# Performance work log

Hardware: AMD Instinct MI355X
Metric: run time of the kernel (lower is better)

Reference implementation:

```python
import math
import jax, jax.numpy as jnp
import numpy as np

B, S, HID = 2, 2048, 4096
H, KV = 32, 8
D = HID // H  # 128


def setup_inputs() -> dict:
    key = jax.random.key(0)
    ks = jax.random.split(key, 6)
    std = 0.02
    x = jax.random.normal(ks[0], (B, S, HID), dtype=jnp.float32)
    # causal additive mask, broadcast over batch and heads
    neg = jnp.full((S, S), -1e9, dtype=jnp.float32)
    mask = jnp.triu(neg, k=1)[None, None, :, :]
    q_w = jax.random.normal(ks[1], (HID, HID), dtype=jnp.float32) * std
    k_w = jax.random.normal(ks[2], (KV * D, HID), dtype=jnp.float32) * std
    v_w = jax.random.normal(ks[3], (KV * D, HID), dtype=jnp.float32) * std
    o_w = jax.random.normal(ks[4], (HID, HID), dtype=jnp.float32) * std
    return {
        "x": x, "mask": mask,
        "q_w": q_w, "q_b": jnp.zeros((HID,), jnp.float32),
        "k_w": k_w, "k_b": jnp.zeros((KV * D,), jnp.float32),
        "v_w": v_w, "v_b": jnp.zeros((KV * D,), jnp.float32),
        "o_w": o_w, "o_b": jnp.zeros((HID,), jnp.float32),
    }


def reference(x, mask, q_w, q_b, k_w, k_b, v_w, v_b, o_w, o_b):
    b, s, _ = x.shape
    rep = H // KV
    # projections (torch Linear convention: y = x @ W^T + b)
    q = (x @ q_w.T + q_b).reshape(b, s, H, D)
    k = (x @ k_w.T + k_b).reshape(b, s, KV, D)
    v = (x @ v_w.T + v_b).reshape(b, s, KV, D)
    # GQA kv-head repeat via concat: q head i attends to kv head (i mod KV)
    k = jnp.concatenate([k] * rep, axis=2)  # [b, s, H, D]
    v = jnp.concatenate([v] * rep, axis=2)
    # [b, H, s, D]
    q = q.transpose(0, 2, 1, 3)
    k = k.transpose(0, 2, 1, 3)
    v = v.transpose(0, 2, 1, 3)
    scores = jnp.einsum("bhqd,bhkd->bhqk", q, k) / math.sqrt(D)
    scores = scores + mask
    w = jax.nn.softmax(scores, axis=-1)
    attn = jnp.einsum("bhqk,bhkd->bhqd", w, v)
    attn = attn.transpose(0, 2, 1, 3).reshape(b, s, HID)
    return attn @ o_w.T + o_b
```

## Files before the change

### kernel.cpp

```cpp
#include <hip/hip_runtime.h>
#include <hip/hip_bf16.h>
#include <cstdint>

typedef __attribute__((ext_vector_type(8))) short s8vec;
typedef __attribute__((ext_vector_type(4))) float f4vec;

#define DEV __device__ __forceinline__

constexpr int Bn = 2, Sn = 2048, HIDn = 4096, Hn = 32, KVn = 8, Dn = 128;

typedef const __attribute__((address_space(1))) void gvoid_t;
typedef __attribute__((address_space(3))) void lvoid_t;

DEV void async_ld16(const void* g, void* l) {
  __builtin_amdgcn_global_load_lds((gvoid_t*)g, (lvoid_t*)l, 16, 0, 0);
}

DEV f4vec mfma16(s8vec a, s8vec b, f4vec c) {
  return __builtin_amdgcn_mfma_f32_16x16x32_bf16(a, b, c, 0, 0, 0);
}

__global__ void cvt_all(const float* __restrict__ x, const float* __restrict__ qw,
                        const float* __restrict__ kw, const float* __restrict__ vw,
                        const float* __restrict__ ow,
                        __hip_bfloat16* __restrict__ xb, __hip_bfloat16* __restrict__ qwb,
                        __hip_bfloat16* __restrict__ kwb, __hip_bfloat16* __restrict__ vwb,
                        __hip_bfloat16* __restrict__ owb) {
  const int i = blockIdx.x * 256 + threadIdx.x;
  const float* src; __hip_bfloat16* dst; int off;
  if (i < 4194304)       { src = x;  dst = xb;  off = i; }
  else if (i < 8388608)  { src = qw; dst = qwb; off = i - 4194304; }
  else if (i < 9437184)  { src = kw; dst = kwb; off = i - 8388608; }
  else if (i < 10485760) { src = vw; dst = vwb; off = i - 9437184; }
  else                   { src = ow; dst = owb; off = i - 10485760; }
  float4 f = ((const float4*)src)[off];
  union { __hip_bfloat16 h[4]; uint2 u; } cv;
  cv.h[0] = __float2bfloat16(f.x);
  cv.h[1] = __float2bfloat16(f.y);
  cv.h[2] = __float2bfloat16(f.z);
  cv.h[3] = __float2bfloat16(f.w);
  ((uint2*)dst)[off] = cv.u;
}

template <typename EpiF>
DEV void gemm_bt_body(const __hip_bfloat16* A, const __hip_bfloat16* Bw, int K,
                      long m0, long n0, EpiF epi) {
  __shared__ __hip_bfloat16 As[128 * 32];
  __shared__ __hip_bfloat16 Bs[128 * 32];
  const int t = threadIdx.x;
  const int w = t >> 6, l = t & 63;
  const int lane15 = l & 15, quad = l >> 4;
  const int wm = (w >> 1) << 6, wn = (w & 1) << 6;

  f4vec acc[4][4] = {};

  const int srow = t >> 2;
  const int scol = (t & 3) << 3;
  const __hip_bfloat16* ag0 = A + (m0 + srow) * (long)K + scol;
  const __hip_bfloat16* ag1 = ag0 + 64 * (long)K;
  const __hip_bfloat16* bg0 = Bw + (n0 + srow) * (long)K + scol;
  const __hip_bfloat16* bg1 = bg0 + 64 * (long)K;
  char* lA = (char*)As + (w << 10);
  char* lB = (char*)Bs + (w << 10);
  const short* Ash = (const short*)As;
  const short* Bsh = (const short*)Bs;
  const int aoff = (wm + lane15) * 32 + (quad << 3);
  const int boff = (wn + lane15) * 32 + (quad << 3);

  for (int k0 = 0; k0 < K; k0 += 32) {
    __syncthreads();
    async_ld16(ag0 + k0, lA);
    async_ld16(ag1 + k0, lA + 4096);
    async_ld16(bg0 + k0, lB);
    async_ld16(bg1 + k0, lB + 4096);
    __syncthreads();
    s8vec af[4], bfr[4];
#pragma unroll
    for (int i = 0; i < 4; i++) {
      af[i] = *(const s8vec*)(Ash + aoff + i * 512);
      bfr[i] = *(const s8vec*)(Bsh + boff + i * 512);
    }
#pragma unroll
    for (int i = 0; i < 4; i++)
#pragma unroll
      for (int j = 0; j < 4; j++)
        acc[i][j] = mfma16(af[i], bfr[j], acc[i][j]);
  }
  epi(acc, wm, wn, lane15, quad);
}

__launch_bounds__(256, 2)
__global__ void gemm_qkv(const __hip_bfloat16* __restrict__ xb,
                         const __hip_bfloat16* __restrict__ qwb,
                         const __hip_bfloat16* __restrict__ kwb,
                         const __hip_bfloat16* __restrict__ vwb,
                         const float* __restrict__ qb, const float* __restrict__ kb,
                         const float* __restrict__ vb,
                         __hip_bfloat16* __restrict__ qh, __hip_bfloat16* __restrict__ kh,
                         __hip_bfloat16* __restrict__ vth) {
  const int bx = blockIdx.x;
  const long m0 = (long)blockIdx.y << 7;
  int mode; long n0;
  const __hip_bfloat16* Bw; const float* bias;
  if (bx < 32)      { mode = 0; Bw = qwb; bias = qb; n0 = (long)bx << 7; }
  else if (bx < 40) { mode = 1; Bw = kwb; bias = kb; n0 = (long)(bx - 32) << 7; }
  else              { mode = 2; Bw = vwb; bias = vb; n0 = (long)(bx - 40) << 7; }

  gemm_bt_body(xb, Bw, 4096, m0, n0,
    [&](f4vec (&acc)[4][4], int wm, int wn, int lane15, int quad) {
      float bv[4];
#pragma unroll
      for (int j = 0; j < 4; j++) bv[j] = bias[n0 + wn + j * 16 + lane15];
#pragma unroll
      for (int i = 0; i < 4; i++)
#pragma unroll
        for (int j = 0; j < 4; j++)
#pragma unroll
          for (int r = 0; r < 4; r++) {
            const long gm = m0 + wm + i * 16 + (quad << 2) + r;
            const long gn = n0 + wn + j * 16 + lane15;
            const float v = acc[i][j][r] + bv[j];
            const long bb = gm >> 11, ss = gm & 2047;
            const long hh = gn >> 7, dd = gn & 127;
            const __hip_bfloat16 hv = __float2bfloat16(v);
            if (mode == 0)
              qh[(((bb * Hn + hh) * Sn + ss) << 7) + dd] = hv;
            else if (mode == 1)
              kh[(((bb * KVn + hh) * Sn + ss) << 7) + dd] = hv;
            else
              vth[((bb * KVn + hh) * Dn + dd) * (long)Sn + ss] = hv;
          }
    });
}

__launch_bounds__(256, 2)
__global__ void gemm_out(const __hip_bfloat16* __restrict__ A,
                         const __hip_bfloat16* __restrict__ Bw,
                         const float* __restrict__ bias, float* __restrict__ Cout) {
  const long m0 = (long)blockIdx.y << 7;
  const long n0 = (long)blockIdx.x << 7;
  gemm_bt_body(A, Bw, 4096, m0, n0,
    [&](f4vec (&acc)[4][4], int wm, int wn, int lane15, int quad) {
      float bv[4];
#pragma unroll
      for (int j = 0; j < 4; j++) bv[j] = bias[n0 + wn + j * 16 + lane15];
#pragma unroll
      for (int i = 0; i < 4; i++)
#pragma unroll
        for (int j = 0; j < 4; j++)
#pragma unroll
          for (int r = 0; r < 4; r++) {
            const long gm = m0 + wm + i * 16 + (quad << 2) + r;
            const long gn = n0 + wn + j * 16 + lane15;
            Cout[gm * HIDn + gn] = acc[i][j][r] + bv[j];
          }
    });
}

__launch_bounds__(256, 2)
__global__ void attn_fused(const __hip_bfloat16* __restrict__ Qh,
                           const __hip_bfloat16* __restrict__ Kh,
                           const __hip_bfloat16* __restrict__ Vt,
                           __hip_bfloat16* __restrict__ Oa) {
  __shared__ __hip_bfloat16 Ks[2][64 * 128];
  __shared__ __hip_bfloat16 Vs[2][128 * 64];
  __shared__ __hip_bfloat16 Ps[4][32 * 64];

  const int pair = blockIdx.x;
  const int h = blockIdx.y;
  const int b = blockIdx.z;
  const int kv = h & 7;

  const int t = threadIdx.x, w = t >> 6, l = t & 63;
  const int lane15 = l & 15, quad = l >> 4;
  const int swz = lane15 & 7;

  const char* KgB = (const char*)(Kh + ((long)(b * KVn + kv)) * Sn * Dn);
  const char* VgB = (const char*)(Vt + ((long)(b * KVn + kv)) * Dn * (long)Sn);

  const int kc = (t & 15) ^ ((t >> 4) & 7);
  const char* kg_base = KgB + (t >> 4) * 256 + kc * 16;
  const int vc = (t & 7) ^ ((t >> 3) & 7);
  const char* vg_base = VgB + (t >> 3) * (size_t)(Sn * 2) + vc * 16;

  const short* Psh = (const short*)Ps[w];
  short* Psw = (short*)Ps[w];
  const float cscale = 0.08838834764831845f * 1.4426950408889634f;
  const float coff = -8.0f * 1.4426950408889634f;

  for (int ph = 0; ph < 2; ph++) {
    const int qt = ph ? (15 - pair) : pair;

    s8vec aq[2][4];
    {
      const short* Qgs = (const short*)(Qh + (((long)(b * Hn + h)) * Sn + qt * 128) * (long)Dn);
#pragma unroll
      for (int i = 0; i < 2; i++)
#pragma unroll
        for (int kk = 0; kk < 4; kk++)
          aq[i][kk] = *(const s8vec*)(Qgs + (w * 32 + i * 16 + lane15) * 128 + kk * 32 + (quad << 3));
    }
    float lsum[2][4] = {};
    f4vec acco[2][8] = {};

    __syncthreads();
    {
      char* lk = (char*)Ks[0] + (w << 10);
      char* lv = (char*)Vs[0] + (w << 10);
#pragma unroll
      for (int i = 0; i < 4; i++) async_ld16(kg_base + i * 4096, lk + i * 4096);
#pragma unroll
      for (int i = 0; i < 4; i++) async_ld16(vg_base + (size_t)i * 32 * Sn * 2, lv + i * 4096);
    }

    const int n_kt = 2 * qt + 2, full_kt = 2 * qt;
    for (int kt = 0; kt < n_kt; kt++) {
      const int cur = kt & 1;
      __syncthreads();
      if (kt + 1 < n_kt) {
        char* lk = (char*)Ks[cur ^ 1] + (w << 10);
        char* lv = (char*)Vs[cur ^ 1] + (w << 10);
        const char* kg = kg_base + (size_t)(kt + 1) * 16384;
        const char* vg = vg_base + (size_t)(kt + 1) * 128;
#pragma unroll
        for (int i = 0; i < 4; i++) async_ld16(kg + i * 4096, lk + i * 4096);
#pragma unroll
        for (int i = 0; i < 4; i++) async_ld16(vg + (size_t)i * 32 * Sn * 2, lv + i * 4096);
      }
      const short* Ksh = (const short*)Ks[cur];
      const short* Vsh = (const short*)Vs[cur];
      const bool need_mask = (kt >= full_kt);

#pragma unroll
      for (int j = 0; j < 4; j++) {
        f4vec as0 = {}, as1 = {};
#pragma unroll
        for (int kk = 0; kk < 4; kk++) {
          const s8vec bk = *(const s8vec*)(Ksh + (j * 16 + lane15) * 128 + (((quad + 4 * kk) ^ swz) << 3));
          as0 = mfma16(aq[0][kk], bk, as0);
          as1 = mfma16(aq[1][kk], bk, as1);
        }
        const int pc = j * 16 + lane15;
        const int kcol = kt * 64 + pc;
#pragma unroll
        for (int i = 0; i < 2; i++) {
#pragma unroll
          for (int r = 0; r < 4; r++) {
            const int pr = i * 16 + (quad << 2) + r;
            float sv = (i ? as1[r] : as0[r]) * cscale + coff;
            if (need_mask) {
              const int qr = qt * 128 + w * 32 + pr;
              if (kcol > qr) sv = -1000000.0f;
            }
            const float p = __builtin_amdgcn_exp2f(sv);
            lsum[i][r] += p;
            Psw[pr * 64 + ((((pc >> 3) ^ (pr & 7)) << 3) | (pc & 7))] =
                __bfloat16_as_short(__float2bfloat16(p));
          }
        }
      }
      asm volatile("s_waitcnt lgkmcnt(0)" ::: "memory");

#pragma unroll
      for (int kk = 0; kk < 2; kk++) {
        s8vec ap[2], bv8[8];
#pragma unroll
        for (int i = 0; i < 2; i++)
          ap[i] = *(const s8vec*)(Psh + (i * 16 + lane15) * 64 + (((quad + 4 * kk) ^ swz) << 3));
#pragma unroll
        for (int j = 0; j < 8; j++)
          bv8[j] = *(const s8vec*)(Vsh + (j * 16 + lane15) * 64 + (((quad + 4 * kk) ^ swz) << 3));
#pragma unroll
        for (int i = 0; i < 2; i++)
#pragma unroll
          for (int j = 0; j < 8; j++)
            acco[i][j] = mfma16(ap[i], bv8[j], acco[i][j]);
      }
    }

#pragma unroll
    for (int i = 0; i < 2; i++)
#pragma unroll
      for (int r = 0; r < 4; r++) {
        float s = lsum[i][r];
#pragma unroll
        for (int d = 1; d < 16; d <<= 1) s += __shfl_xor(s, d);
        lsum[i][r] = 1.0f / s;
      }
#pragma unroll
    for (int i = 0; i < 2; i++) {
#pragma unroll
      for (int r = 0; r < 4; r++) {
        const int row = qt * 128 + w * 32 + i * 16 + (quad << 2) + r;
        const long base = ((long)b * Sn + row) * HIDn + h * Dn;
#pragma unroll
        for (int j = 0; j < 8; j++)
          Oa[base + j * 16 + lane15] = __float2bfloat16(acco[i][j][r] * lsum[i][r]);
      }
    }
  }
}

extern "C" void kernel_launch(void* const* d_in, const int* in_sizes, int n_in,
                              void* d_out, int out_size, void* d_ws, size_t ws_size,
                              hipStream_t stream) {
  const float* x   = (const float*)d_in[0];
  const float* q_w = (const float*)d_in[2];
  const float* q_b = (const float*)d_in[3];
  const float* k_w = (const float*)d_in[4];
  const float* k_b = (const float*)d_in[5];
  const float* v_w = (const float*)d_in[6];
  const float* v_b = (const float*)d_in[7];
  const float* o_w = (const float*)d_in[8];
  const float* o_b = (const float*)d_in[9];

  char* ws = (char*)d_ws;
  size_t off = 0;
  auto nxt = [&](size_t bytes) { char* p = ws + off; off += bytes; return p; };
  __hip_bfloat16* xb  = (__hip_bfloat16*)nxt(33554432);
  __hip_bfloat16* qwb = (__hip_bfloat16*)nxt(33554432);
  __hip_bfloat16* kwb = (__hip_bfloat16*)nxt(8388608);
  __hip_bfloat16* vwb = (__hip_bfloat16*)nxt(8388608);
  __hip_bfloat16* owb = (__hip_bfloat16*)nxt(33554432);
  __hip_bfloat16* qh  = (__hip_bfloat16*)nxt(33554432);
  __hip_bfloat16* kh  = (__hip_bfloat16*)nxt(8388608);
  __hip_bfloat16* vth = (__hip_bfloat16*)nxt(8388608);
  __hip_bfloat16* at  = (__hip_bfloat16*)nxt(33554432);
  (void)ws_size; (void)in_sizes; (void)n_in; (void)out_size;

  cvt_all<<<57344, 256, 0, stream>>>(x, q_w, k_w, v_w, o_w, xb, qwb, kwb, vwb, owb);
  gemm_qkv<<<dim3(48, 32), 256, 0, stream>>>(xb, qwb, kwb, vwb, q_b, k_b, v_b, qh, kh, vth);
  attn_fused<<<dim3(8, 32, 2), 256, 0, stream>>>(qh, kh, vth, at);
  gemm_out<<<dim3(32, 32), 256, 0, stream>>>(at, owb, o_b, (float*)d_out);
}
```

Baseline: 743.2 us.

## Triple-buffer GEMM mainloop with 256x128 tiles, swizzled LDS and async prefetch

Reworks the shared GEMM body used by the QKV and output projections. It uses 256x128 block tiles with 8 waves and a K-step of 64, and stages operands into three LDS buffers via async global-to-LDS loads issued two iterations ahead. Synchronisation uses explicit vmcnt waits and a single barrier per step, and an XOR swizzle on LDS columns avoids bank conflicts. The aim is to hide global load latency and cut barrier overhead. In exchange, the large LDS footprint limits occupancy to one block per CU.

New measurement: 728.3 us. 2.0% less time.

```diff
diff --git a/kernel.cpp b/kernel.cpp
--- a/kernel.cpp
+++ b/kernel.cpp
@@ -45,51 +45,96 @@
 template <typename EpiF>
 DEV void gemm_bt_body(const __hip_bfloat16* A, const __hip_bfloat16* Bw, int K,
                       long m0, long n0, EpiF epi) {
-  __shared__ __hip_bfloat16 As[128 * 32];
-  __shared__ __hip_bfloat16 Bs[128 * 32];
+  __shared__ __hip_bfloat16 As[3][256 * 64];
+  __shared__ __hip_bfloat16 Bs[3][128 * 64];
   const int t = threadIdx.x;
   const int w = t >> 6, l = t & 63;
   const int lane15 = l & 15, quad = l >> 4;
-  const int wm = (w >> 1) << 6, wn = (w & 1) << 6;
+  const int wm = (w >> 1) << 6;
+  const int wn = (w & 1) << 6;
 
   f4vec acc[4][4] = {};
 
-  const int srow = t >> 2;
-  const int scol = (t & 3) << 3;
-  const __hip_bfloat16* ag0 = A + (m0 + srow) * (long)K + scol;
-  const __hip_bfloat16* ag1 = ag0 + 64 * (long)K;
-  const __hip_bfloat16* bg0 = Bw + (n0 + srow) * (long)K + scol;
-  const __hip_bfloat16* bg1 = bg0 + 64 * (long)K;
-  char* lA = (char*)As + (w << 10);
-  char* lB = (char*)Bs + (w << 10);
-  const short* Ash = (const short*)As;
-  const short* Bsh = (const short*)Bs;
-  const int aoff = (wm + lane15) * 32 + (quad << 3);
-  const int boff = (wn + lane15) * 32 + (quad << 3);
-
-  for (int k0 = 0; k0 < K; k0 += 32) {
-    __syncthreads();
-    async_ld16(ag0 + k0, lA);
-    async_ld16(ag1 + k0, lA + 4096);
-    async_ld16(bg0 + k0, lB);
-    async_ld16(bg1 + k0, lB + 4096);
-    __syncthreads();
-    s8vec af[4], bfr[4];
-#pragma unroll
-    for (int i = 0; i < 4; i++) {
-      af[i] = *(const s8vec*)(Ash + aoff + i * 512);
-      bfr[i] = *(const s8vec*)(Bsh + boff + i * 512);
-    }
+  const int col_e = ((l & 7) << 3) ^ (((l >> 5) & 1) << 4);
+  const __hip_bfloat16* agA = A + (m0 + w * 8 + (l >> 3)) * (long)K + col_e;
+  const __hip_bfloat16* agB = Bw + (n0 + w * 8 + (l >> 3)) * (long)K + col_e;
+  const long rowK64 = (long)K << 6;
+
+  auto stageA = [&](int buf, int kt, int i) {
+    async_ld16(agA + (long)i * rowK64 + ((long)kt << 6),
+               (char*)(As[buf]) + ((i * 8 + w) << 10));
+  };
+  auto stageB = [&](int buf, int kt, int i) {
+    async_ld16(agB + (long)i * rowK64 + ((long)kt << 6),
+               (char*)(Bs[buf]) + ((i * 8 + w) << 10));
+  };
+
+  const int colxor = (lane15 & 4) << 3;
+  const int cq = (quad << 4) ^ colxor;
+  int arow[4], brow[4];
+#pragma unroll
+  for (int i = 0; i < 4; i++) arow[i] = (wm + i * 16 + lane15) << 7;
+#pragma unroll
+  for (int j = 0; j < 4; j++) brow[j] = (wn + j * 16 + lane15) << 7;
+
+  const int NT = K >> 6;
+
+#pragma unroll
+  for (int i = 0; i < 4; i++) stageA(0, 0, i);
+#pragma unroll
+  for (int i = 0; i < 2; i++) stageB(0, 0, i);
+#pragma unroll
+  for (int i = 0; i < 4; i++) stageA(1, 1, i);
+#pragma unroll
+  for (int i = 0; i < 2; i++) stageB(1, 1, i);
+  asm volatile("s_waitcnt vmcnt(6)" ::: "memory");
+  __builtin_amdgcn_s_barrier();
+  __builtin_amdgcn_sched_barrier(0);
+
+  int bi = 0, nb = 2;
+  for (int tau = 0; tau < NT; ++tau) {
+    const char* Ab = (const char*)As[bi];
+    const char* Bb = (const char*)Bs[bi];
+    const bool st = (tau + 2) < NT;
+    s8vec af[4], bf4[4];
+
+#pragma unroll
+    for (int i = 0; i < 4; i++) af[i] = *(const s8vec*)(Ab + arow[i] + cq);
+#pragma unroll
+    for (int j = 0; j < 4; j++) bf4[j] = *(const s8vec*)(Bb + brow[j] + cq);
+    if (st) { stageA(nb, tau + 2, 0); stageA(nb, tau + 2, 1); stageB(nb, tau + 2, 0); }
+    __builtin_amdgcn_s_setprio(1);
 #pragma unroll
     for (int i = 0; i < 4; i++)
 #pragma unroll
-      for (int j = 0; j < 4; j++)
-        acc[i][j] = mfma16(af[i], bfr[j], acc[i][j]);
+      for (int j = 0; j < 4; j++) acc[i][j] = mfma16(af[i], bf4[j], acc[i][j]);
+    __builtin_amdgcn_s_setprio(0);
+
+#pragma unroll
+    for (int i = 0; i < 4; i++) af[i] = *(const s8vec*)(Ab + arow[i] + cq + 64);
+#pragma unroll
+    for (int j = 0; j < 4; j++) bf4[j] = *(const s8vec*)(Bb + brow[j] + cq + 64);
+    if (st) { stageA(nb, tau + 2, 2); stageA(nb, tau + 2, 3); stageB(nb, tau + 2, 1); }
+    __builtin_amdgcn_s_setprio(1);
+#pragma unroll
+    for (int i = 0; i < 4; i++)
+#pragma unroll
+      for (int j = 0; j < 4; j++) acc[i][j] = mfma16(af[i], bf4[j], acc[i][j]);
+    __builtin_amdgcn_s_setprio(0);
+
+    if (tau + 1 < NT) {
+      if (st) asm volatile("s_waitcnt vmcnt(6)" ::: "memory");
+      else    asm volatile("s_waitcnt vmcnt(0)" ::: "memory");
+      __builtin_amdgcn_s_barrier();
+      __builtin_amdgcn_sched_barrier(0);
+    }
+    bi = (bi + 1 == 3) ? 0 : bi + 1;
+    nb = (nb + 1 == 3) ? 0 : nb + 1;
   }
   epi(acc, wm, wn, lane15, quad);
 }
 
-__launch_bounds__(256, 2)
+__launch_bounds__(512, 2)
 __global__ void gemm_qkv(const __hip_bfloat16* __restrict__ xb,
                          const __hip_bfloat16* __restrict__ qwb,
                          const __hip_bfloat16* __restrict__ kwb,
@@ -99,7 +144,7 @@
                          __hip_bfloat16* __restrict__ qh, __hip_bfloat16* __restrict__ kh,
                          __hip_bfloat16* __restrict__ vth) {
   const int bx = blockIdx.x;
-  const long m0 = (long)blockIdx.y << 7;
+  const long m0 = (long)blockIdx.y << 8;
   int mode; long n0;
   const __hip_bfloat16* Bw; const float* bias;
   if (bx < 32)      { mode = 0; Bw = qwb; bias = qb; n0 = (long)bx << 7; }
@@ -133,11 +178,11 @@
     });
 }
 
-__launch_bounds__(256, 2)
+__launch_bounds__(512, 2)
 __global__ void gemm_out(const __hip_bfloat16* __restrict__ A,
                          const __hip_bfloat16* __restrict__ Bw,
                          const float* __restrict__ bias, float* __restrict__ Cout) {
-  const long m0 = (long)blockIdx.y << 7;
+  const long m0 = (long)blockIdx.y << 8;
   const long n0 = (long)blockIdx.x << 7;
   gemm_bt_body(A, Bw, 4096, m0, n0,
     [&](f4vec (&acc)[4][4], int wm, int wn, int lane15, int quad) {
@@ -329,7 +374,7 @@
   (void)ws_size; (void)in_sizes; (void)n_in; (void)out_size;
 
   cvt_all<<<57344, 256, 0, stream>>>(x, q_w, k_w, v_w, o_w, xb, qwb, kwb, vwb, owb);
-  gemm_qkv<<<dim3(48, 32), 256, 0, stream>>>(xb, qwb, kwb, vwb, q_b, k_b, v_b, qh, kh, vth);
+  gemm_qkv<<<dim3(48, 16), 512, 0, stream>>>(xb, qwb, kwb, vwb, q_b, k_b, v_b, qh, kh, vth);
   attn_fused<<<dim3(8, 32, 2), 256, 0, stream>>>(qh, kh, vth, at);
-  gemm_out<<<dim3(32, 32), 256, 0, stream>>>(at, owb, o_b, (float*)d_out);
-}
+  gemm_out<<<dim3(32, 16), 512, 0, stream>>>(at, owb, o_b, (float*)d_out);
+}
```
